# Kernel tuning notes

Hardware: AMD Instinct MI355X
Metric: run time of the kernel (lower is better)

## Reference

```python
import jax, jax.numpy as jnp
import numpy as np

B, W, LOCAL, GLOBAL = 32, 16, 64, 64
EMB, HIDDEN, OUT, NLAYERS = 256, 512, 64, 3
T = 128  # output_len


def setup_inputs() -> dict:
    key = jax.random.key(0)
    ks = jax.random.split(key, 16)
    s = 0.05
    inp = {
        "z_t": jax.random.normal(ks[0], (B, W, LOCAL), jnp.float32),
        "z_g": jax.random.normal(ks[1], (B, GLOBAL), jnp.float32),
        # embedding: Linear(local+global -> 256, bias=False), torch layout (out,in)
        "w_emb": jax.random.normal(ks[2], (EMB, LOCAL + GLOBAL), jnp.float32) * s,
        # GRU(input_size=1, hidden=256); input is all-zeros so w_ih contributes
        # nothing (only its bias b_ih matters) -> faithfully omit w_ih.
        "gru_w_hh": jax.random.normal(ks[3], (3 * EMB, EMB), jnp.float32) * s,
        "gru_b_ih": jax.random.normal(ks[4], (3 * EMB,), jnp.float32) * s,
        "gru_b_hh": jax.random.normal(ks[5], (3 * EMB,), jnp.float32) * s,
        "mlp_w1": jax.random.normal(ks[6], (HIDDEN, EMB), jnp.float32) * s,
        "mlp_b1": jax.random.normal(ks[7], (HIDDEN,), jnp.float32) * s,
        "mlp_w2": jax.random.normal(ks[8], (HIDDEN, HIDDEN), jnp.float32) * s,
        "mlp_b2": jax.random.normal(ks[9], (HIDDEN,), jnp.float32) * s,
        "mlp_w3": jax.random.normal(ks[10], (HIDDEN, HIDDEN), jnp.float32) * s,
        "mlp_b3": jax.random.normal(ks[11], (HIDDEN,), jnp.float32) * s,
        "mu_w": jax.random.normal(ks[12], (OUT, HIDDEN), jnp.float32) * s,
        "mu_b": jax.random.normal(ks[13], (OUT,), jnp.float32) * s,
        "output_len": T,
    }
    return inp


def _gru_zero_input(h0, w_hh, b_ih, b_hh, length):
    # PyTorch GRU cell with x_t == 0: input-to-hidden term reduces to b_ih.
    b_ir, b_iz, b_in = jnp.split(b_ih, 3)

    def step(h, _):
        gh = h @ w_hh.T + b_hh              # (BW, 3*EMB)
        g_r, g_z, g_n = jnp.split(gh, 3, axis=-1)
        r = jax.nn.sigmoid(b_ir + g_r)
        z = jax.nn.sigmoid(b_iz + g_z)
        n = jnp.tanh(b_in + r * g_n)
        h_new = (1.0 - z) * n + z * h
        return h_new, h_new

    _, hs = jax.lax.scan(step, h0, None, length=length)
    return hs  # (T, BW, EMB)


def reference(z_t, z_g, w_emb, gru_w_hh, gru_b_ih, gru_b_hh,
              mlp_w1, mlp_b1, mlp_w2, mlp_b2, mlp_w3, mlp_b3,
              mu_w, mu_b, output_len):
    b, nw, _ = z_t.shape
    z = jnp.concatenate(
        [z_t, jnp.broadcast_to(z_g[:, None, :], (b, nw, z_g.shape[-1]))], axis=-1)
    emb = z @ w_emb.T                        # (B, W, EMB)
    h0 = emb.reshape(b * nw, -1)             # (BW, EMB) initial hidden state

    hs = _gru_zero_input(h0, gru_w_hh, gru_b_ih, gru_b_hh, output_len)
    h_t = jnp.transpose(hs, (1, 0, 2))       # (BW, T, EMB), batch_first

    # MLP: Linear+ELU (Dropout p=0.05 is identity in eval)
    h = jax.nn.elu(h_t @ mlp_w1.T + mlp_b1)
    h = jax.nn.elu(h @ mlp_w2.T + mlp_b2)
    h = jax.nn.elu(h @ mlp_w3.T + mlp_b3)
    x_mean = h @ mu_w.T + mu_b               # (BW, T, OUT)
    return x_mean.reshape(b, nw * output_len, -1)
```

## Files before the change

kernel.cpp:

```cpp
#include <hip/hip_runtime.h>
#include <hip/hip_bf16.h>


typedef __bf16 bf16_t;
typedef __bf16 bf16x2 __attribute__((ext_vector_type(2)));
typedef __bf16 bf16x8 __attribute__((ext_vector_type(8)));
typedef float f32x4 __attribute__((ext_vector_type(4)));

#define MFMA16(a, b, c) __builtin_amdgcn_mfma_f32_16x16x32_bf16(a, b, c, 0, 0, 0)

#define EMB 256
#define TSTEPS 128
#define OUTD 64

#define HS_OFF   0u
#define H0_OFF   33554432u
#define WHH_OFF  34078720u
#define W1_OFF   34471936u
#define W2_OFF   34734080u
#define W3_OFF   35258368u
#define MUW_OFF  35782656u

__device__ __forceinline__ float rcpf(float x){ return __builtin_amdgcn_rcpf(x); }
__device__ __forceinline__ void lds_barrier() {
  asm volatile("s_waitcnt lgkmcnt(0)\n\ts_barrier" ::: "memory");
}

__global__ __launch_bounds__(256) void convert_kernel(
    const float* __restrict__ whh, const float* __restrict__ w1,
    const float* __restrict__ w2, const float* __restrict__ w3,
    const float* __restrict__ muw, char* __restrict__ ws)
{
  const int g = blockIdx.x * 256 + threadIdx.x;
  const int G = gridDim.x * 256;
  bf16_t* d;
  d = (bf16_t*)(ws + WHH_OFF); for (int i = g; i < 196608; i += G) d[i] = (bf16_t)whh[i];
  d = (bf16_t*)(ws + W1_OFF);  for (int i = g; i < 131072; i += G) d[i] = (bf16_t)w1[i];
  d = (bf16_t*)(ws + W2_OFF);  for (int i = g; i < 262144; i += G) d[i] = (bf16_t)w2[i];
  d = (bf16_t*)(ws + W3_OFF);  for (int i = g; i < 262144; i += G) d[i] = (bf16_t)w3[i];
  d = (bf16_t*)(ws + MUW_OFF); for (int i = g; i < 32768;  i += G) d[i] = (bf16_t)muw[i];
}

__global__ __launch_bounds__(256) void emb_kernel(
    const float* __restrict__ z_t, const float* __restrict__ z_g,
    const float* __restrict__ w_emb, float* __restrict__ h0)
{
  __shared__ float zrow[128];
  const int bw = blockIdx.x, tid = threadIdx.x;
  if (tid < 128)
    zrow[tid] = (tid < 64) ? z_t[bw * 64 + tid] : z_g[(bw >> 4) * 64 + (tid - 64)];
  __syncthreads();
  const float4* wp = reinterpret_cast<const float4*>(w_emb + (size_t)tid * 128);
  float s = 0.f;
#pragma unroll
  for (int k4 = 0; k4 < 32; ++k4) {
    const float4 w = wp[k4];
    s += zrow[k4 * 4 + 0] * w.x + zrow[k4 * 4 + 1] * w.y
       + zrow[k4 * 4 + 2] * w.z + zrow[k4 * 4 + 3] * w.w;
  }
  h0[(size_t)bw * 256 + tid] = s;
}

__global__ __launch_bounds__(512) void gru_kernel(
    const float* __restrict__ h0, const bf16_t* __restrict__ w_hh,
    const float* __restrict__ b_ih, const float* __restrict__ b_hh,
    bf16_t* __restrict__ hs)
{
  __shared__ __align__(16) float  gh[4][772];
  __shared__ __align__(16) bf16_t h16[16][264];

  const int tid  = threadIdx.x;
  const int wv   = tid >> 6;
  const int lane = tid & 63;
  const int l15  = lane & 15;
  const int quad = lane >> 4;
  const int bw0  = blockIdx.x * 4;

  bf16x8 wfrag[6][8];
#pragma unroll
  for (int ct = 0; ct < 6; ++ct) {
    const int n = wv * 96 + ct * 16 + l15;
#pragma unroll
    for (int kk = 0; kk < 8; ++kk)
      wfrag[ct][kk] = *reinterpret_cast<const bf16x8*>(w_hh + (size_t)n * 256 + kk * 32 + quad * 8);
  }

  const int grow = tid >> 7;
  const int c0   = (tid * 2) & 255;
  float br[2], bz[2], bin[2], bhn[2], hm[2];
#pragma unroll
  for (int j = 0; j < 2; ++j) {
    const int c = c0 + j;
    br[j]  = b_ih[c]       + b_hh[c];
    bz[j]  = b_ih[256 + c] + b_hh[256 + c];
    bin[j] = b_ih[512 + c];
    bhn[j] = b_hh[512 + c];
    hm[j]  = h0[(size_t)(bw0 + grow) * 256 + c];
  }
  {
    bf16x2 v; v[0] = (bf16_t)hm[0]; v[1] = (bf16_t)hm[1];
    *reinterpret_cast<bf16x2*>(&h16[grow][c0]) = v;
    for (int i = tid; i < 12 * 132; i += 512) {
      const int rr = 4 + (i / 132), cc = (i % 132) * 2;
      *reinterpret_cast<bf16x2*>(&h16[rr][cc]) = bf16x2{(bf16_t)0.f, (bf16_t)0.f};
    }
  }
  __syncthreads();

#pragma unroll 1
  for (int t = 0; t < TSTEPS; ++t) {
    f32x4 acc[6] = {};
#pragma unroll
    for (int kk = 0; kk < 8; ++kk) {
      bf16x8 a = *reinterpret_cast<const bf16x8*>(&h16[l15][kk * 32 + quad * 8]);
#pragma unroll
      for (int ct = 0; ct < 6; ++ct)
        acc[ct] = MFMA16(a, wfrag[ct][kk], acc[ct]);
    }
    if (quad == 0) {
#pragma unroll
      for (int ct = 0; ct < 6; ++ct) {
        const int n = wv * 96 + ct * 16 + l15;
#pragma unroll
        for (int r = 0; r < 4; ++r) gh[r][n] = acc[ct][r];
      }
    }
    lds_barrier();

    bf16_t nh[2];
#pragma unroll
    for (int j = 0; j < 2; ++j) {
      const int c = c0 + j;
      const float gr = gh[grow][c]       + br[j];
      const float gz = gh[grow][256 + c] + bz[j];
      const float gn = gh[grow][512 + c] + bhn[j];
      const float rr = rcpf(1.f + __expf(-gr));
      const float zz = rcpf(1.f + __expf(-gz));
      const float pre = bin[j] + rr * gn;
      const float nn = 1.f - 2.f * rcpf(__expf(2.f * pre) + 1.f);
      hm[j] = nn + zz * (hm[j] - nn);
      nh[j] = (bf16_t)hm[j];
    }
    {
      bf16x2 v; v[0] = nh[0]; v[1] = nh[1];
      *reinterpret_cast<bf16x2*>(&h16[grow][c0]) = v;
      *reinterpret_cast<bf16x2*>(hs + ((size_t)(bw0 + grow) * TSTEPS + t) * EMB + c0) = v;
    }
    lds_barrier();
  }
}

template<int KC>
__device__ __forceinline__ void mlp_layer(
    const bf16_t* __restrict__ W, const float* __restrict__ bias,
    bf16_t (*act)[520], int wv, int l15, int quad)
{
  f32x4 acc[4][8] = {};
#pragma unroll 2
  for (int kc = 0; kc < KC; ++kc) {
#pragma unroll
    for (int kk = 0; kk < 4; ++kk) {
      bf16x8 wf[4];
#pragma unroll
      for (int ct = 0; ct < 4; ++ct)
        wf[ct] = *reinterpret_cast<const bf16x8*>(
            W + (size_t)(wv * 64 + ct * 16 + l15) * (KC * 128) + kc * 128 + kk * 32 + quad * 8);
#pragma unroll
      for (int mt = 0; mt < 8; ++mt) {
        bf16x8 a = *reinterpret_cast<const bf16x8*>(&act[mt * 16 + l15][kc * 128 + kk * 32 + quad * 8]);
#pragma unroll
        for (int ct = 0; ct < 4; ++ct)
          acc[ct][mt] = MFMA16(a, wf[ct], acc[ct][mt]);
      }
    }
  }
  __syncthreads();
#pragma unroll
  for (int ct = 0; ct < 4; ++ct) {
    const int n = wv * 64 + ct * 16 + l15;
    const float b = bias[n];
#pragma unroll
    for (int mt = 0; mt < 8; ++mt)
#pragma unroll
      for (int r = 0; r < 4; ++r) {
        float x = acc[ct][mt][r] + b;
        x = (x > 0.f) ? x : (__expf(x) - 1.f);
        act[mt * 16 + quad * 4 + r][n] = (bf16_t)x;
      }
  }
  __syncthreads();
}

__global__ __launch_bounds__(512, 2) void mlp_kernel(
    const bf16_t* __restrict__ hs,
    const bf16_t* __restrict__ w1, const float* __restrict__ b1,
    const bf16_t* __restrict__ w2, const float* __restrict__ b2,
    const bf16_t* __restrict__ w3, const float* __restrict__ b3,
    const bf16_t* __restrict__ muw, const float* __restrict__ mub,
    float* __restrict__ out)
{
  __shared__ __align__(16) bf16_t act[128][520];

  const int tid  = threadIdx.x;
  const int wv   = tid >> 6;
  const int lane = tid & 63;
  const int l15  = lane & 15;
  const int quad = lane >> 4;
  const size_t r0 = (size_t)blockIdx.x * 128;

  for (int v = tid; v < 128 * 32; v += 512) {
    const int rr = v >> 5, cc = v & 31;
    bf16x8 x = *reinterpret_cast<const bf16x8*>(hs + (r0 + rr) * EMB + cc * 8);
    *reinterpret_cast<bf16x8*>(&act[rr][cc * 8]) = x;
  }
  __syncthreads();

  mlp_layer<2>(w1, b1, act, wv, l15, quad);
  mlp_layer<4>(w2, b2, act, wv, l15, quad);
  mlp_layer<4>(w3, b3, act, wv, l15, quad);

  f32x4 macc[4] = {};
  const int n   = (wv & 3) * 16 + l15;
  const int mtb = (wv >> 2) * 4;
#pragma unroll 1
  for (int kc = 0; kc < 4; ++kc) {
#pragma unroll
    for (int kk = 0; kk < 4; ++kk) {
      bf16x8 wf = *reinterpret_cast<const bf16x8*>(
          muw + (size_t)n * 512 + kc * 128 + kk * 32 + quad * 8);
#pragma unroll
      for (int i = 0; i < 4; ++i) {
        bf16x8 a = *reinterpret_cast<const bf16x8*>(
            &act[(mtb + i) * 16 + l15][kc * 128 + kk * 32 + quad * 8]);
        macc[i] = MFMA16(a, wf, macc[i]);
      }
    }
  }
  const float mb = mub[n];
#pragma unroll
  for (int i = 0; i < 4; ++i)
#pragma unroll
    for (int r = 0; r < 4; ++r)
      out[(r0 + (mtb + i) * 16 + quad * 4 + r) * OUTD + n] = macc[i][r] + mb;
}

extern "C" void kernel_launch(void* const* d_in, const int* in_sizes, int n_in,
                              void* d_out, int out_size, void* d_ws, size_t ws_size,
                              hipStream_t stream) {
  char* ws = (char*)d_ws;

  convert_kernel<<<256, 256, 0, stream>>>(
      (const float*)d_in[3], (const float*)d_in[6], (const float*)d_in[8],
      (const float*)d_in[10], (const float*)d_in[12], ws);

  emb_kernel<<<512, 256, 0, stream>>>(
      (const float*)d_in[0], (const float*)d_in[1], (const float*)d_in[2],
      (float*)(ws + H0_OFF));

  gru_kernel<<<128, 512, 0, stream>>>(
      (const float*)(ws + H0_OFF), (const bf16_t*)(ws + WHH_OFF),
      (const float*)d_in[4], (const float*)d_in[5],
      (bf16_t*)(ws + HS_OFF));

  mlp_kernel<<<512, 512, 0, stream>>>(
      (const bf16_t*)(ws + HS_OFF),
      (const bf16_t*)(ws + W1_OFF), (const float*)d_in[7],
      (const bf16_t*)(ws + W2_OFF), (const float*)d_in[9],
      (const bf16_t*)(ws + W3_OFF), (const float*)d_in[11],
      (const bf16_t*)(ws + MUW_OFF), (const float*)d_in[13],
      (float*)d_out);
}
```

Baseline: 392.2 us.

## Restructure GRU step so gates stay in registers with double-buffered hidden state

The GRU kernel now uses 4 waves instead of 8, and each wave holds 12 weight column tiles covering its r, z and n gate columns. Each lane can then compute the gate update straight from MFMA accumulators, with no round trip through a shared gate buffer. The hidden state is double-buffered in LDS, which cuts the per-step barriers from two to one. The cost is higher register pressure (96 bf16x8 weight fragments per lane), half the waves per block, and scattered 2-byte stores to hs.

Result: faster. 372.0 us (-5.1%).

```diff
diff --git a/kernel.cpp b/kernel.cpp
--- a/kernel.cpp
+++ b/kernel.cpp
@@ -61,13 +61,12 @@
   h0[(size_t)bw * 256 + tid] = s;
 }
 
-__global__ __launch_bounds__(512) void gru_kernel(
+__global__ __launch_bounds__(256, 1) void gru_kernel(
     const float* __restrict__ h0, const bf16_t* __restrict__ w_hh,
     const float* __restrict__ b_ih, const float* __restrict__ b_hh,
     bf16_t* __restrict__ hs)
 {
-  __shared__ __align__(16) float  gh[4][772];
-  __shared__ __align__(16) bf16_t h16[16][264];
+  __shared__ __align__(16) bf16_t h16[2][16][264];
 
   const int tid  = threadIdx.x;
   const int wv   = tid >> 6;
@@ -75,76 +74,71 @@
   const int l15  = lane & 15;
   const int quad = lane >> 4;
   const int bw0  = blockIdx.x * 4;
-
-  bf16x8 wfrag[6][8];
-#pragma unroll
-  for (int ct = 0; ct < 6; ++ct) {
-    const int n = wv * 96 + ct * 16 + l15;
+  const int c0   = wv * 16 + l15;
+
+  bf16x8 wfrag[12][8];
+#pragma unroll
+  for (int ct = 0; ct < 12; ++ct) {
+    const int n = (ct >> 2) * 256 + (ct & 3) * 64 + c0;
 #pragma unroll
     for (int kk = 0; kk < 8; ++kk)
-      wfrag[ct][kk] = *reinterpret_cast<const bf16x8*>(w_hh + (size_t)n * 256 + kk * 32 + quad * 8);
-  }
-
-  const int grow = tid >> 7;
-  const int c0   = (tid * 2) & 255;
-  float br[2], bz[2], bin[2], bhn[2], hm[2];
-#pragma unroll
-  for (int j = 0; j < 2; ++j) {
-    const int c = c0 + j;
+      wfrag[ct][kk] = *reinterpret_cast<const bf16x8*>(
+          w_hh + (size_t)n * 256 + kk * 32 + quad * 8);
+  }
+
+  float br[4], bz[4], bin[4], bhn[4], hm[4];
+#pragma unroll
+  for (int j = 0; j < 4; ++j) {
+    const int c = c0 + j * 64;
     br[j]  = b_ih[c]       + b_hh[c];
     bz[j]  = b_ih[256 + c] + b_hh[256 + c];
     bin[j] = b_ih[512 + c];
     bhn[j] = b_hh[512 + c];
-    hm[j]  = h0[(size_t)(bw0 + grow) * 256 + c];
-  }
+    hm[j]  = h0[(size_t)(bw0 + quad) * 256 + c];
+  }
+
   {
-    bf16x2 v; v[0] = (bf16_t)hm[0]; v[1] = (bf16_t)hm[1];
-    *reinterpret_cast<bf16x2*>(&h16[grow][c0]) = v;
-    for (int i = tid; i < 12 * 132; i += 512) {
-      const int rr = 4 + (i / 132), cc = (i % 132) * 2;
-      *reinterpret_cast<bf16x2*>(&h16[rr][cc]) = bf16x2{(bf16_t)0.f, (bf16_t)0.f};
-    }
-  }
-  __syncthreads();
+    bf16x8 zv;
+#pragma unroll
+    for (int e = 0; e < 8; ++e) zv[e] = (bf16_t)0.f;
+    for (int i = tid; i < 1056; i += 256)
+      reinterpret_cast<bf16x8*>(h16)[i] = zv;
+  }
+  __syncthreads();
+#pragma unroll
+  for (int j = 0; j < 4; ++j)
+    h16[0][quad * 4][c0 + j * 64] = (bf16_t)hm[j];
+  __syncthreads();
+
+  bf16_t* hsp = hs + ((size_t)(bw0 + quad) * TSTEPS) * EMB + c0;
 
 #pragma unroll 1
   for (int t = 0; t < TSTEPS; ++t) {
-    f32x4 acc[6] = {};
+    const bf16_t (*hr)[264] = h16[t & 1];
+    bf16_t (*hw)[264] = h16[(t & 1) ^ 1];
+
+    f32x4 acc[12] = {};
 #pragma unroll
     for (int kk = 0; kk < 8; ++kk) {
-      bf16x8 a = *reinterpret_cast<const bf16x8*>(&h16[l15][kk * 32 + quad * 8]);
-#pragma unroll
-      for (int ct = 0; ct < 6; ++ct)
+      const bf16x8 a = *reinterpret_cast<const bf16x8*>(&hr[l15][kk * 32 + quad * 8]);
+#pragma unroll
+      for (int ct = 0; ct < 12; ++ct)
         acc[ct] = MFMA16(a, wfrag[ct][kk], acc[ct]);
     }
-    if (quad == 0) {
-#pragma unroll
-      for (int ct = 0; ct < 6; ++ct) {
-        const int n = wv * 96 + ct * 16 + l15;
-#pragma unroll
-        for (int r = 0; r < 4; ++r) gh[r][n] = acc[ct][r];
-      }
-    }
-    lds_barrier();
-
-    bf16_t nh[2];
-#pragma unroll
-    for (int j = 0; j < 2; ++j) {
-      const int c = c0 + j;
-      const float gr = gh[grow][c]       + br[j];
-      const float gz = gh[grow][256 + c] + bz[j];
-      const float gn = gh[grow][512 + c] + bhn[j];
+
+#pragma unroll
+    for (int j = 0; j < 4; ++j) {
+      const float gr = acc[j][0]     + br[j];
+      const float gz = acc[4 + j][0] + bz[j];
+      const float gn = acc[8 + j][0] + bhn[j];
       const float rr = rcpf(1.f + __expf(-gr));
       const float zz = rcpf(1.f + __expf(-gz));
       const float pre = bin[j] + rr * gn;
       const float nn = 1.f - 2.f * rcpf(__expf(2.f * pre) + 1.f);
       hm[j] = nn + zz * (hm[j] - nn);
-      nh[j] = (bf16_t)hm[j];
-    }
-    {
-      bf16x2 v; v[0] = nh[0]; v[1] = nh[1];
-      *reinterpret_cast<bf16x2*>(&h16[grow][c0]) = v;
-      *reinterpret_cast<bf16x2*>(hs + ((size_t)(bw0 + grow) * TSTEPS + t) * EMB + c0) = v;
+      const bf16_t nh = (bf16_t)hm[j];
+      hw[quad * 4][c0 + j * 64] = nh;
+      hsp[(size_t)t * EMB + j * 64] = nh;
     }
     lds_barrier();
   }
@@ -257,7 +251,7 @@
       (const float*)d_in[0], (const float*)d_in[1], (const float*)d_in[2],
       (float*)(ws + H0_OFF));
 
-  gru_kernel<<<128, 512, 0, stream>>>(
+  gru_kernel<<<128, 256, 0, stream>>>(
       (const float*)(ws + H0_OFF), (const bf16_t*)(ws + WHH_OFF),
       (const float*)d_in[4], (const float*)d_in[5],
       (bf16_t*)(ws + HS_OFF));
```
